# Optimization experiments

Measured on AMD Instinct MI355X. Metric: run time of the kernel, lower is better.

## Reference

```python
import jax, jax.numpy as jnp
import numpy as np
import math

IMG, P, C, D, DEPTH, H, MLP, NCLS, B = 224, 16, 3, 768, 12, 12, 3072, 1000, 32
G = IMG // P          # 14 patches per side
N = G * G             # 196 patches
S = N + 1             # 197 tokens (cls + patches)
DK = D // H
PD = P * P * C        # 768 flattened patch dim


def layer_norm(x, g, b, eps=1e-5):
    mu = jnp.mean(x, axis=-1, keepdims=True)
    var = jnp.mean((x - mu) ** 2, axis=-1, keepdims=True)
    return (x - mu) * jax.lax.rsqrt(var + eps) * g + b


def setup_inputs() -> dict:
    key = jax.random.key(0)
    ks = iter(jax.random.split(key, 32))
    nrm = lambda shape, s=0.02: jax.random.normal(next(ks), shape, jnp.float32) * s
    inp = {
        'x': jax.random.normal(next(ks), (B, C, IMG, IMG), jnp.float32),
        'patch_W': nrm((PD, D)), 'patch_b': jnp.zeros((D,)),
        'cls_token': nrm((1, 1, D)), 'pos_embed': nrm((1, S, D)),
        'Wq': nrm((DEPTH, D, D)), 'bq': jnp.zeros((DEPTH, D)),
        'Wk': nrm((DEPTH, D, D)), 'bk': jnp.zeros((DEPTH, D)),
        'Wv': nrm((DEPTH, D, D)), 'bv': jnp.zeros((DEPTH, D)),
        'Wo': nrm((DEPTH, D, D)), 'bo': jnp.zeros((DEPTH, D)),
        'ln1_g': jnp.ones((DEPTH, D)), 'ln1_b': jnp.zeros((DEPTH, D)),
        'ln2_g': jnp.ones((DEPTH, D)), 'ln2_b': jnp.zeros((DEPTH, D)),
        'W1': nrm((DEPTH, D, MLP)), 'b1': jnp.zeros((DEPTH, MLP)),
        'W2': nrm((DEPTH, MLP, D)), 'b2': jnp.zeros((DEPTH, D)),
        'lnp_g': jnp.ones((D,)), 'lnp_b': jnp.zeros((D,)),
        'head_W': nrm((D, NCLS)), 'head_b': jnp.zeros((NCLS,)),
    }
    return inp


def vit_forward(x, patch_W, patch_b, cls_token, pos_embed,
                Wq, bq, Wk, bk, Wv, bv, Wo, bo,
                ln1_g, ln1_b, ln2_g, ln2_b, W1, b1, W2, b2,
                lnp_g, lnp_b, head_W, head_b):
    b = x.shape[0]
    # faithful replication of torch unfold(2).unfold(3).view: (B,C,G,P,G,P)->(B,C,G,G,P,P)->row-major flatten
    patches = x.reshape(b, C, G, P, G, P).transpose(0, 1, 2, 4, 3, 5).reshape(b, N, PD)
    h = patches @ patch_W + patch_b                              # [B,N,D]
    h = jnp.concatenate([jnp.broadcast_to(cls_token, (b, 1, D)), h], axis=1) + pos_embed
    scale = 1.0 / math.sqrt(DK)
    for i in range(DEPTH):
        y = layer_norm(h, ln1_g[i], ln1_b[i])
        q = (y @ Wq[i] + bq[i]).reshape(b, S, H, DK).transpose(0, 2, 1, 3)
        k = (y @ Wk[i] + bk[i]).reshape(b, S, H, DK).transpose(0, 2, 1, 3)
        v = (y @ Wv[i] + bv[i]).reshape(b, S, H, DK).transpose(0, 2, 1, 3)
        attn = jax.nn.softmax(jnp.einsum('bhqd,bhkd->bhqk', q, k) * scale, axis=-1)
        att = jnp.einsum('bhqk,bhkd->bhqd', attn, v).transpose(0, 2, 1, 3).reshape(b, S, D)
        h = h + att @ Wo[i] + bo[i]
        y = layer_norm(h, ln2_g[i], ln2_b[i])
        h = h + jax.nn.gelu(y @ W1[i] + b1[i], approximate=False) @ W2[i] + b2[i]
    h = layer_norm(h, lnp_g, lnp_b)
    return h[:, 0] @ head_W + head_b                              # [B, NCLS]


def reference(x, patch_W, patch_b, cls_token, pos_embed,
              Wq, bq, Wk, bk, Wv, bv, Wo, bo,
              ln1_g, ln1_b, ln2_g, ln2_b, W1, b1, W2, b2,
              lnp_g, lnp_b, head_W, head_b):
    return vit_forward(x, patch_W, patch_b, cls_token, pos_embed,
                       Wq, bq, Wk, bk, Wv, bv, Wo, bo,
                       ln1_g, ln1_b, ln2_g, ln2_b, W1, b1, W2, b2,
                       lnp_g, lnp_b, head_W, head_b)
```

## Files before the change

### kernel.cpp

```cpp
#include <hip/hip_runtime.h>
#include <hip/hip_bf16.h>


typedef __attribute__((ext_vector_type(8))) short short8;
typedef __attribute__((ext_vector_type(4))) float f32x4;
typedef __attribute__((ext_vector_type(4))) unsigned short us4;

#define MFMA16(a, b, c) __builtin_amdgcn_mfma_f32_16x16x32_bf16(a, b, c, 0, 0, 0)

#define BATCH 32
#define SEQ 197
#define SPAD 208
#define DIM 768
#define HEADS 12
#define DKH 64
#define MLPD 3072
#define NCLS 1000
#define NPATCH 196
#define PDIM 768
#define QKVD 2304
#define ROWS (BATCH * SPAD)

static __device__ __forceinline__ unsigned short f2bf(float f) {
    unsigned int u = __builtin_bit_cast(unsigned int, f);
    u += 0x7fffu + ((u >> 16) & 1u);
    return (unsigned short)(u >> 16);
}

__device__ __forceinline__ void gload16(const void* g, void* l) {
    __builtin_amdgcn_global_load_lds(
        (const __attribute__((address_space(1))) void*)g,
        (__attribute__((address_space(3))) void*)l, 16, 0, 0);
}

__global__ __launch_bounds__(256) void patchify(const float* __restrict__ x,
                                                unsigned short* __restrict__ out) {
    int i = blockIdx.x * 256 + threadIdx.x;
    if (i >= BATCH * NPATCH * PDIM) return;
    int b = i / (NPATCH * PDIM);
    int f = i % (NPATCH * PDIM);
    int c = f / 50176, r = f % 50176;
    int gy = r / 3584, r2 = r % 3584;
    int gx = r2 >> 8, r3 = r2 & 255;
    int py = r3 >> 4, px = r3 & 15;
    float v = x[(((size_t)b * 3 + c) * 224 + gy * 16 + py) * 224 + gx * 16 + px];
    out[i] = f2bf(v);
}

__global__ __launch_bounds__(256) void embed_misc(const float* __restrict__ cls,
                                                  const float* __restrict__ pos,
                                                  float* __restrict__ h) {
    int b = blockIdx.x, t = threadIdx.x;
    float* hb = h + (size_t)b * SPAD * DIM;
    for (int d = t; d < DIM; d += 256) hb[d] = cls[d] + pos[d];
    for (int i = t; i < (SPAD - SEQ) * DIM; i += 256) hb[SEQ * DIM + i] = 0.f;
}

__global__ __launch_bounds__(256) void tconv(const float* __restrict__ src,
                                             unsigned short* __restrict__ dst,
                                             int K, int N) {
    __shared__ float tile[32][33];
    int tn = blockIdx.x, tk = blockIdx.y;
    int t = threadIdx.x, r = t >> 3, c4 = (t & 7) << 2;
    float4 v = *reinterpret_cast<const float4*>(&src[(size_t)(tk * 32 + r) * N + tn * 32 + c4]);
    tile[r][c4 + 0] = v.x; tile[r][c4 + 1] = v.y;
    tile[r][c4 + 2] = v.z; tile[r][c4 + 3] = v.w;
    __syncthreads();
    us4 o = { f2bf(tile[c4 + 0][r]), f2bf(tile[c4 + 1][r]),
              f2bf(tile[c4 + 2][r]), f2bf(tile[c4 + 3][r]) };
    *reinterpret_cast<us4*>(&dst[(size_t)(tn * 32 + r) * K + tk * 32 + c4]) = o;
}

__global__ __launch_bounds__(256) void hconv(const float* __restrict__ src,
                                             unsigned short* __restrict__ dst) {
    __shared__ float tile[32][33];
    int tn = blockIdx.x, tk = blockIdx.y;
    int t = threadIdx.x, r = t >> 3, c4 = (t & 7) << 2;
#pragma unroll
    for (int i = 0; i < 4; ++i) {
        int c = tn * 32 + c4 + i;
        tile[r][c4 + i] = (c < NCLS) ? src[(size_t)(tk * 32 + r) * NCLS + c] : 0.f;
    }
    __syncthreads();
    us4 o = { f2bf(tile[c4 + 0][r]), f2bf(tile[c4 + 1][r]),
              f2bf(tile[c4 + 2][r]), f2bf(tile[c4 + 3][r]) };
    *reinterpret_cast<us4*>(&dst[(size_t)(tn * 32 + r) * 768 + tk * 32 + c4]) = o;
}

__global__ __launch_bounds__(256) void wconvert(const float* __restrict__ q,
                                                const float* __restrict__ k,
                                                const float* __restrict__ v,
                                                const float* __restrict__ o,
                                                const float* __restrict__ w1,
                                                const float* __restrict__ w2,
                                                unsigned short* __restrict__ wT) {
    __shared__ float tile[32][33];
    int tb = blockIdx.x;
    const float* src; unsigned short* dst; int K, N;
    if (tb < 2304) {
        K = 768; N = 768;
        int m = tb / 576; tb -= m * 576;
        src = (m == 0) ? q : (m == 1) ? k : (m == 2) ? v : o;
        dst = wT + (m < 3 ? (size_t)m * 589824 : (size_t)1769472);
    } else if (tb < 4608) {
        tb -= 2304; K = 768; N = 3072; src = w1; dst = wT + 2359296;
    } else {
        tb -= 4608; K = 3072; N = 768; src = w2; dst = wT + 4718592;
    }
    int TN = N >> 5;
    int tn = tb % TN, tk = tb / TN;
    int t = threadIdx.x, r = t >> 3, c4 = (t & 7) << 2;
    float4 vv = *reinterpret_cast<const float4*>(&src[(size_t)(tk * 32 + r) * N + tn * 32 + c4]);
    tile[r][c4 + 0] = vv.x; tile[r][c4 + 1] = vv.y;
    tile[r][c4 + 2] = vv.z; tile[r][c4 + 3] = vv.w;
    __syncthreads();
    us4 ov = { f2bf(tile[c4 + 0][r]), f2bf(tile[c4 + 1][r]),
               f2bf(tile[c4 + 2][r]), f2bf(tile[c4 + 3][r]) };
    *reinterpret_cast<us4*>(&dst[(size_t)(tn * 32 + r) * K + tk * 32 + c4]) = ov;
}

__global__ __launch_bounds__(256) void pack_bias(const float* __restrict__ bq,
                                                 const float* __restrict__ bk,
                                                 const float* __restrict__ bv,
                                                 float* __restrict__ dst) {
    int i = blockIdx.x * 256 + threadIdx.x;
    if (i >= 12 * QKVD) return;
    int l = i / QKVD, c = i % QKVD;
    float v = (c < 768) ? bq[l * 768 + c]
            : (c < 1536) ? bk[l * 768 + c - 768]
                         : bv[l * 768 + c - 1536];
    dst[i] = v;
}

template <int BM>
__global__ __launch_bounds__(256) void gemm_tn(
    const unsigned short* __restrict__ A, const unsigned short* __restrict__ Bt,
    const float* __restrict__ bias, int M, int N, int K, int mode,
    unsigned short* __restrict__ outb, float* __restrict__ outf,
    const float* __restrict__ pos) {
    constexpr int MFRAG = BM / 32;
    constexpr int ACH = BM / 8;
    constexpr int TOT = ACH + 16;
    constexpr int CPW = TOT / 4;
    __shared__ unsigned short Alds[BM * 64];
    __shared__ unsigned short Blds[128 * 64];
    const int tid = threadIdx.x, lane = tid & 63, wid = tid >> 6;
    const int row0 = blockIdx.x * BM, col0 = blockIdx.y * 128;
    const int wm = (wid >> 1) * (BM / 2), wn = (wid & 1) * 64;
    const int lr = lane & 15, lg = lane >> 4;
    const int ric = lane >> 3;
    const int sswz = (lane & 7) ^ ric;

    const char* gptr[CPW];
    char* lptr[CPW];
#pragma unroll
    for (int j = 0; j < CPW; ++j) {
        int cc = wid * CPW + j;
        if (cc < ACH) {
            int grow = row0 + cc * 8 + ric;
            gptr[j] = (const char*)A + (size_t)grow * K * 2 + sswz * 16;
            lptr[j] = (char*)Alds + cc * 1024;
        } else {
            int grow = col0 + (cc - ACH) * 8 + ric;
            gptr[j] = (const char*)Bt + (size_t)grow * K * 2 + sswz * 16;
            lptr[j] = (char*)Blds + (cc - ACH) * 1024;
        }
    }

    f32x4 acc[MFRAG][4];
#pragma unroll
    for (int m = 0; m < MFRAG; ++m)
#pragma unroll
        for (int n = 0; n < 4; ++n) acc[m][n] = (f32x4){0.f, 0.f, 0.f, 0.f};

    const int rsw = lr & 7;
    for (int ks = 0; ks < K; ks += 64) {
        __syncthreads();
#pragma unroll
        for (int j = 0; j < CPW; ++j) {
            gload16(gptr[j], lptr[j]);
            gptr[j] += 128;
        }
        __syncthreads();
        short8 af[MFRAG][2], bfr[4][2];
#pragma unroll
        for (int m = 0; m < MFRAG; ++m)
#pragma unroll
            for (int kk = 0; kk < 2; ++kk)
                af[m][kk] = *reinterpret_cast<const short8*>(
                    &Alds[(wm + m * 16 + lr) * 64 + (((kk * 4 + lg) ^ rsw) << 3)]);
#pragma unroll
        for (int n = 0; n < 4; ++n)
#pragma unroll
            for (int kk = 0; kk < 2; ++kk)
                bfr[n][kk] = *reinterpret_cast<const short8*>(
                    &Blds[(wn + n * 16 + lr) * 64 + (((kk * 4 + lg) ^ rsw) << 3)]);
#pragma unroll
        for (int m = 0; m < MFRAG; ++m)
#pragma unroll
            for (int n = 0; n < 4; ++n) {
                acc[m][n] = MFMA16(af[m][0], bfr[n][0], acc[m][n]);
                acc[m][n] = MFMA16(af[m][1], bfr[n][1], acc[m][n]);
            }
    }
#pragma unroll
    for (int m = 0; m < MFRAG; ++m) {
#pragma unroll
        for (int n = 0; n < 4; ++n) {
            int gcol = col0 + wn + n * 16 + lr;
            float bv = bias ? bias[gcol] : 0.f;
#pragma unroll
            for (int i = 0; i < 4; ++i) {
                int grow = row0 + wm + m * 16 + lg * 4 + i;
                float v = acc[m][n][i] + bv;
                if (mode == 0) {
                    outb[(size_t)grow * N + gcol] = f2bf(v);
                } else if (mode == 1) {
                    outf[(size_t)grow * N + gcol] += v;
                } else if (mode == 2) {
                    v = 0.5f * v * (1.f + erff(v * 0.70710678118654752f));
                    outb[(size_t)grow * N + gcol] = f2bf(v);
                } else if (mode == 3) {
                    int pb = grow / NPATCH, pn = grow % NPATCH;
                    size_t o = ((size_t)pb * SPAD + 1 + pn) * DIM + gcol;
                    outf[o] = v + pos[(size_t)(1 + pn) * DIM + gcol];
                } else {
                    if (grow < BATCH && gcol < NCLS)
                        outf[(size_t)grow * NCLS + gcol] = v + pos[gcol];
                }
            }
        }
    }
}

__global__ __launch_bounds__(256) void ln_bf16(const float* __restrict__ x,
                                               const float* __restrict__ g,
                                               const float* __restrict__ b,
                                               unsigned short* __restrict__ y) {
    __shared__ float red[8];
    int row = blockIdx.x, t = threadIdx.x;
    const float* xr = x + (size_t)row * DIM;
    float v0 = xr[t], v1 = xr[t + 256], v2 = xr[t + 512];
    float s = v0 + v1 + v2, sq = v0 * v0 + v1 * v1 + v2 * v2;
#pragma unroll
    for (int off = 1; off < 64; off <<= 1) {
        s += __shfl_xor(s, off);
        sq += __shfl_xor(sq, off);
    }
    if ((t & 63) == 0) { red[t >> 6] = s; red[4 + (t >> 6)] = sq; }
    __syncthreads();
    s = red[0] + red[1] + red[2] + red[3];
    sq = red[4] + red[5] + red[6] + red[7];
    float mu = s * (1.f / 768.f);
    float var = fmaxf(sq * (1.f / 768.f) - mu * mu, 0.f);
    float rs = rsqrtf(var + 1e-5f);
    unsigned short* yr = y + (size_t)row * DIM;
    yr[t]       = f2bf((v0 - mu) * rs * g[t] + b[t]);
    yr[t + 256] = f2bf((v1 - mu) * rs * g[t + 256] + b[t + 256]);
    yr[t + 512] = f2bf((v2 - mu) * rs * g[t + 512] + b[t + 512]);
}

__global__ __launch_bounds__(256) void ln_cls(const float* __restrict__ x,
                                              const float* __restrict__ g,
                                              const float* __restrict__ b,
                                              unsigned short* __restrict__ y) {
    __shared__ float red[8];
    int bb = blockIdx.x, t = threadIdx.x;
    unsigned short* yr = y + (size_t)bb * DIM;
    if (bb >= BATCH) {
        yr[t] = 0; yr[t + 256] = 0; yr[t + 512] = 0;
        return;
    }
    const float* xr = x + (size_t)bb * SPAD * DIM;
    float v0 = xr[t], v1 = xr[t + 256], v2 = xr[t + 512];
    float s = v0 + v1 + v2, sq = v0 * v0 + v1 * v1 + v2 * v2;
#pragma unroll
    for (int off = 1; off < 64; off <<= 1) {
        s += __shfl_xor(s, off);
        sq += __shfl_xor(sq, off);
    }
    if ((t & 63) == 0) { red[t >> 6] = s; red[4 + (t >> 6)] = sq; }
    __syncthreads();
    s = red[0] + red[1] + red[2] + red[3];
    sq = red[4] + red[5] + red[6] + red[7];
    float mu = s * (1.f / 768.f);
    float var = fmaxf(sq * (1.f / 768.f) - mu * mu, 0.f);
    float rs = rsqrtf(var + 1e-5f);
    yr[t]       = f2bf((v0 - mu) * rs * g[t] + b[t]);
    yr[t + 256] = f2bf((v1 - mu) * rs * g[t + 256] + b[t + 256]);
    yr[t + 512] = f2bf((v2 - mu) * rs * g[t + 512] + b[t + 512]);
}

__global__ __launch_bounds__(256) void attn_fused(const unsigned short* __restrict__ qkv,
                                                  unsigned short* __restrict__ att) {
    __shared__ unsigned short Vlds[64][232];
    __shared__ unsigned short Plds[4][16 * 256];
    int h = blockIdx.x, b = blockIdx.y, tid = threadIdx.x;
    for (int idx = tid; idx < SPAD * 8; idx += 256) {
        int s = idx >> 3, dc = (idx & 7) << 3;
        uint4 w = *reinterpret_cast<const uint4*>(
            &qkv[((size_t)b * SPAD + s) * QKVD + 1536 + h * DKH + dc]);
        const unsigned short* pe = reinterpret_cast<const unsigned short*>(&w);
#pragma unroll
        for (int i = 0; i < 8; ++i) Vlds[dc + i][s] = pe[i];
    }
    for (int i = tid; i < 64 * 24; i += 256) Vlds[i / 24][208 + (i % 24)] = 0;
    __syncthreads();

    int wid = tid >> 6, lane = tid & 63, lr = lane & 15, lg = lane >> 4;
    unsigned short* Pw = &Plds[wid][0];
    const short8 zero8 = {0, 0, 0, 0, 0, 0, 0, 0};

    for (int qt = wid; qt < 13; qt += 4) {
        size_t qoff = ((size_t)b * SPAD + qt * 16 + lr) * QKVD + h * DKH + lg * 8;
        short8 qf0 = *reinterpret_cast<const short8*>(&qkv[qoff]);
        short8 qf1 = *reinterpret_cast<const short8*>(&qkv[qoff + 32]);
        f32x4 acc[13];
#pragma unroll
        for (int kt = 0; kt < 13; ++kt) {
            size_t koff = ((size_t)b * SPAD + kt * 16 + lr) * QKVD + 768 + h * DKH + lg * 8;
            short8 kf0 = *reinterpret_cast<const short8*>(&qkv[koff]);
            short8 kf1 = *reinterpret_cast<const short8*>(&qkv[koff + 32]);
            f32x4 a = (f32x4){0.f, 0.f, 0.f, 0.f};
            a = MFMA16(qf0, kf0, a);
            a = MFMA16(qf1, kf1, a);
            acc[kt] = a;
        }
#pragma unroll
        for (int kt = 0; kt < 13; ++kt)
#pragma unroll
            for (int r = 0; r < 4; ++r) acc[kt][r] *= 0.125f;
        if (lr >= 5) {
#pragma unroll
            for (int r = 0; r < 4; ++r) acc[12][r] = -1e30f;
        }
        float mx[4] = {-1e30f, -1e30f, -1e30f, -1e30f};
#pragma unroll
        for (int kt = 0; kt < 13; ++kt)
#pragma unroll
            for (int r = 0; r < 4; ++r) mx[r] = fmaxf(mx[r], acc[kt][r]);
#pragma unroll
        for (int r = 0; r < 4; ++r) {
            mx[r] = fmaxf(mx[r], __shfl_xor(mx[r], 1));
            mx[r] = fmaxf(mx[r], __shfl_xor(mx[r], 2));
            mx[r] = fmaxf(mx[r], __shfl_xor(mx[r], 4));
            mx[r] = fmaxf(mx[r], __shfl_xor(mx[r], 8));
        }
        float sm[4] = {0.f, 0.f, 0.f, 0.f};
#pragma unroll
        for (int kt = 0; kt < 13; ++kt)
#pragma unroll
            for (int r = 0; r < 4; ++r) {
                float e = __expf(acc[kt][r] - mx[r]);
                acc[kt][r] = e;
                sm[r] += e;
            }
#pragma unroll
        for (int r = 0; r < 4; ++r) {
            sm[r] += __shfl_xor(sm[r], 1);
            sm[r] += __shfl_xor(sm[r], 2);
            sm[r] += __shfl_xor(sm[r], 4);
            sm[r] += __shfl_xor(sm[r], 8);
        }
#pragma unroll
        for (int r = 0; r < 4; ++r) {
            int row = lg * 4 + r;
            float inv = 1.f / sm[r];
#pragma unroll
            for (int kt = 0; kt < 13; ++kt) {
                int col = kt * 16 + lr;
                int idx = row * 256 + ((((col >> 3) ^ (row & 7)) << 3) | (col & 7));
                Pw[idx] = f2bf(acc[kt][r] * inv);
            }
        }
        if (lr < 6) {
            int s = 26 + lr;
#pragma unroll
            for (int r = 0; r < 4; ++r) {
                int row = lg * 4 + r;
                *reinterpret_cast<short8*>(&Pw[row * 256 + ((s ^ (row & 7)) << 3)]) = zero8;
            }
        }
        int rsw = lr & 7;
#pragma unroll
        for (int dt = 0; dt < 4; ++dt) {
            f32x4 a = (f32x4){0.f, 0.f, 0.f, 0.f};
#pragma unroll
            for (int kk = 0; kk < 7; ++kk) {
                short8 af = *reinterpret_cast<const short8*>(
                    &Pw[lr * 256 + (((kk * 4 + lg) ^ rsw) << 3)]);
                short8 bfr = *reinterpret_cast<const short8*>(
                    &Vlds[dt * 16 + lr][kk * 32 + lg * 8]);
                a = MFMA16(af, bfr, a);
            }
#pragma unroll
            for (int i = 0; i < 4; ++i) {
                int s = qt * 16 + lg * 4 + i;
                att[((size_t)b * SPAD + s) * DIM + h * DKH + dt * 16 + lr] = f2bf(a[i]);
            }
        }
    }
}

extern "C" void kernel_launch(void* const* d_in, const int* in_sizes, int n_in,
                              void* d_out, int out_size, void* d_ws, size_t ws_size,
                              hipStream_t stream) {
    const float* x      = (const float*)d_in[0];
    const float* patchW = (const float*)d_in[1];
    const float* patchB = (const float*)d_in[2];
    const float* clstok = (const float*)d_in[3];
    const float* pose   = (const float*)d_in[4];
    const float* Wq = (const float*)d_in[5];
    const float* bq = (const float*)d_in[6];
    const float* Wk = (const float*)d_in[7];
    const float* bk = (const float*)d_in[8];
    const float* Wv = (const float*)d_in[9];
    const float* bv = (const float*)d_in[10];
    const float* Wo = (const float*)d_in[11];
    const float* bo = (const float*)d_in[12];
    const float* ln1g = (const float*)d_in[13];
    const float* ln1b = (const float*)d_in[14];
    const float* ln2g = (const float*)d_in[15];
    const float* ln2b = (const float*)d_in[16];
    const float* W1 = (const float*)d_in[17];
    const float* b1 = (const float*)d_in[18];
    const float* W2 = (const float*)d_in[19];
    const float* b2 = (const float*)d_in[20];
    const float* lnpg = (const float*)d_in[21];
    const float* lnpb = (const float*)d_in[22];
    const float* headW = (const float*)d_in[23];
    const float* headB = (const float*)d_in[24];
    float* out = (float*)d_out;

    constexpr size_t SZ_H   = (size_t)ROWS * DIM * 4;
    constexpr size_t SZ_QKV = (size_t)ROWS * QKVD * 2;
    constexpr size_t SZ_Y   = (size_t)ROWS * DIM * 2;
    constexpr size_t SZ_M1  = (size_t)ROWS * MLPD * 2;
    constexpr size_t SZ_WT  = (size_t)7077888 * 2;
    char* w = (char*)d_ws;
    float* hbuf            = (float*)w;
    unsigned short* qkvb   = (unsigned short*)(w + SZ_H);
    unsigned short* ybuf   = (unsigned short*)(w + SZ_H + SZ_QKV);
    unsigned short* m1buf  = (unsigned short*)(w + SZ_H + SZ_QKV + SZ_Y);
    unsigned short* wT     = (unsigned short*)(w + SZ_H + SZ_QKV + SZ_Y + SZ_M1);
    float* bqkv            = (float*)(w + SZ_H + SZ_QKV + SZ_Y + SZ_M1 + SZ_WT);
    unsigned short* patches = m1buf;
    unsigned short* clsbuf  = m1buf;
    unsigned short* hwT     = m1buf + 64 * DIM;

    pack_bias<<<dim3(108), 256, 0, stream>>>(bq, bk, bv, bqkv);

    tconv<<<dim3(24, 24), 256, 0, stream>>>(patchW, wT, PDIM, DIM);
    patchify<<<dim3((BATCH * NPATCH * PDIM + 255) / 256), 256, 0, stream>>>(x, patches);
    embed_misc<<<dim3(BATCH), 256, 0, stream>>>(clstok, pose, hbuf);
    gemm_tn<64><<<dim3(98, 6), 256, 0, stream>>>(patches, wT, patchB,
                                                 BATCH * NPATCH, DIM, PDIM, 3,
                                                 nullptr, hbuf, pose);

    for (int i = 0; i < 12; ++i) {
        const size_t wo = (size_t)i * DIM * DIM;
        const size_t wm = (size_t)i * DIM * MLPD;
        wconvert<<<dim3(6912), 256, 0, stream>>>(Wq + wo, Wk + wo, Wv + wo, Wo + wo,
                                                 W1 + wm, W2 + wm, wT);
        ln_bf16<<<dim3(ROWS), 256, 0, stream>>>(hbuf, ln1g + i * DIM, ln1b + i * DIM, ybuf);
        gemm_tn<128><<<dim3(52, 18), 256, 0, stream>>>(ybuf, wT, bqkv + i * QKVD,
                                                       ROWS, QKVD, DIM, 0,
                                                       qkvb, nullptr, nullptr);
        attn_fused<<<dim3(HEADS, BATCH), 256, 0, stream>>>(qkvb, ybuf);
        gemm_tn<64><<<dim3(104, 6), 256, 0, stream>>>(ybuf, wT + 1769472, bo + i * DIM,
                                                      ROWS, DIM, DIM, 1,
                                                      nullptr, hbuf, nullptr);
        ln_bf16<<<dim3(ROWS), 256, 0, stream>>>(hbuf, ln2g + i * DIM, ln2b + i * DIM, ybuf);
        gemm_tn<128><<<dim3(52, 24), 256, 0, stream>>>(ybuf, wT + 2359296, b1 + i * MLPD,
                                                       ROWS, MLPD, DIM, 2,
                                                       m1buf, nullptr, nullptr);
        gemm_tn<64><<<dim3(104, 6), 256, 0, stream>>>(m1buf, wT + 4718592, b2 + i * DIM,
                                                      ROWS, DIM, MLPD, 1,
                                                      nullptr, hbuf, nullptr);
    }
    ln_cls<<<dim3(64), 256, 0, stream>>>(hbuf, lnpg, lnpb, clsbuf);
    hconv<<<dim3(32, 24), 256, 0, stream>>>(headW, hwT);
    gemm_tn<64><<<dim3(1, 8), 256, 0, stream>>>(clsbuf, hwT, nullptr,
                                                64, 1024, DIM, 4,
                                                nullptr, out, headB);
}
```

Measured before the change: 3.260 ms.

## Double-buffer GEMM LDS tiles and enlarge block tiles to 128x256 with 8 waves

The GEMM kernel now uses double-buffered shared memory, prefetching the next K-slab while computing on the current one. This removes one barrier per iteration and hides global load latency. Tiles change to a fixed 128-row M tile with a BN of 128 or 256 and 4 or 8 waves, so the QKV and MLP1 GEMMs run 512-thread blocks with 128x256 tiles and the other GEMMs use 128x128. Shared memory use rises, which may lower occupancy, and the head GEMM and ln_cls are resized to match the 128-row tile.

```diff
diff --git a/kernel.cpp b/kernel.cpp
--- a/kernel.cpp
+++ b/kernel.cpp
@@ -132,79 +132,96 @@
     dst[i] = v;
 }
 
-template <int BM>
-__global__ __launch_bounds__(256) void gemm_tn(
+template <int BN, int NW>
+__global__ __launch_bounds__(64 * NW) void gemm_tn(
     const unsigned short* __restrict__ A, const unsigned short* __restrict__ Bt,
     const float* __restrict__ bias, int M, int N, int K, int mode,
     unsigned short* __restrict__ outb, float* __restrict__ outf,
     const float* __restrict__ pos) {
-    constexpr int MFRAG = BM / 32;
-    constexpr int ACH = BM / 8;
-    constexpr int TOT = ACH + 16;
-    constexpr int CPW = TOT / 4;
-    __shared__ unsigned short Alds[BM * 64];
-    __shared__ unsigned short Blds[128 * 64];
+    constexpr int NWN = NW / 2;
+    constexpr int ACH = 16;
+    constexpr int BCH = BN / 8;
+    constexpr int TOT = ACH + BCH;
+    constexpr int CPW = TOT / NW;
+    constexpr int ASZ = 128 * 64;
+    constexpr int BSZ = BN * 64;
+    __shared__ unsigned short Alds[2 * ASZ];
+    __shared__ unsigned short Blds[2 * BSZ];
     const int tid = threadIdx.x, lane = tid & 63, wid = tid >> 6;
-    const int row0 = blockIdx.x * BM, col0 = blockIdx.y * 128;
-    const int wm = (wid >> 1) * (BM / 2), wn = (wid & 1) * 64;
+    const int row0 = blockIdx.x * 128, col0 = blockIdx.y * BN;
+    const int wm = (wid / NWN) * 64, wn = (wid % NWN) * 64;
     const int lr = lane & 15, lg = lane >> 4;
     const int ric = lane >> 3;
     const int sswz = (lane & 7) ^ ric;
 
     const char* gptr[CPW];
-    char* lptr[CPW];
+    char* l0[CPW];
+    int ldelta[CPW];
 #pragma unroll
     for (int j = 0; j < CPW; ++j) {
         int cc = wid * CPW + j;
         if (cc < ACH) {
             int grow = row0 + cc * 8 + ric;
             gptr[j] = (const char*)A + (size_t)grow * K * 2 + sswz * 16;
-            lptr[j] = (char*)Alds + cc * 1024;
+            l0[j] = (char*)Alds + cc * 1024;
+            ldelta[j] = ASZ * 2;
         } else {
             int grow = col0 + (cc - ACH) * 8 + ric;
             gptr[j] = (const char*)Bt + (size_t)grow * K * 2 + sswz * 16;
-            lptr[j] = (char*)Blds + (cc - ACH) * 1024;
-        }
-    }
-
-    f32x4 acc[MFRAG][4];
-#pragma unroll
-    for (int m = 0; m < MFRAG; ++m)
+            l0[j] = (char*)Blds + (cc - ACH) * 1024;
+            ldelta[j] = BSZ * 2;
+        }
+    }
+
+    f32x4 acc[4][4];
+#pragma unroll
+    for (int m = 0; m < 4; ++m)
 #pragma unroll
         for (int n = 0; n < 4; ++n) acc[m][n] = (f32x4){0.f, 0.f, 0.f, 0.f};
 
+#pragma unroll
+    for (int j = 0; j < CPW; ++j) {
+        gload16(gptr[j], l0[j]);
+        gptr[j] += 128;
+    }
+
     const int rsw = lr & 7;
+    int buf = 0;
     for (int ks = 0; ks < K; ks += 64) {
         __syncthreads();
-#pragma unroll
-        for (int j = 0; j < CPW; ++j) {
-            gload16(gptr[j], lptr[j]);
-            gptr[j] += 128;
-        }
-        __syncthreads();
-        short8 af[MFRAG][2], bfr[4][2];
-#pragma unroll
-        for (int m = 0; m < MFRAG; ++m)
+        if (ks + 64 < K) {
+#pragma unroll
+            for (int j = 0; j < CPW; ++j) {
+                gload16(gptr[j], l0[j] + (buf ^ 1) * ldelta[j]);
+                gptr[j] += 128;
+            }
+        }
+        const unsigned short* Ab = Alds + buf * ASZ;
+        const unsigned short* Bb = Blds + buf * BSZ;
+        short8 af[4][2], bfr[4][2];
+#pragma unroll
+        for (int m = 0; m < 4; ++m)
 #pragma unroll
             for (int kk = 0; kk < 2; ++kk)
                 af[m][kk] = *reinterpret_cast<const short8*>(
-                    &Alds[(wm + m * 16 + lr) * 64 + (((kk * 4 + lg) ^ rsw) << 3)]);
+                    &Ab[(wm + m * 16 + lr) * 64 + (((kk * 4 + lg) ^ rsw) << 3)]);
 #pragma unroll
         for (int n = 0; n < 4; ++n)
 #pragma unroll
             for (int kk = 0; kk < 2; ++kk)
                 bfr[n][kk] = *reinterpret_cast<const short8*>(
-                    &Blds[(wn + n * 16 + lr) * 64 + (((kk * 4 + lg) ^ rsw) << 3)]);
-#pragma unroll
-        for (int m = 0; m < MFRAG; ++m)
+                    &Bb[(wn + n * 16 + lr) * 64 + (((kk * 4 + lg) ^ rsw) << 3)]);
+#pragma unroll
+        for (int m = 0; m < 4; ++m)
 #pragma unroll
             for (int n = 0; n < 4; ++n) {
                 acc[m][n] = MFMA16(af[m][0], bfr[n][0], acc[m][n]);
                 acc[m][n] = MFMA16(af[m][1], bfr[n][1], acc[m][n]);
             }
-    }
-#pragma unroll
-    for (int m = 0; m < MFRAG; ++m) {
+        buf ^= 1;
+    }
+#pragma unroll
+    for (int m = 0; m < 4; ++m) {
 #pragma unroll
         for (int n = 0; n < 4; ++n) {
             int gcol = col0 + wn + n * 16 + lr;
@@ -446,16 +463,16 @@
     float* bqkv            = (float*)(w + SZ_H + SZ_QKV + SZ_Y + SZ_M1 + SZ_WT);
     unsigned short* patches = m1buf;
     unsigned short* clsbuf  = m1buf;
-    unsigned short* hwT     = m1buf + 64 * DIM;
+    unsigned short* hwT     = m1buf + 128 * DIM;
 
     pack_bias<<<dim3(108), 256, 0, stream>>>(bq, bk, bv, bqkv);
 
     tconv<<<dim3(24, 24), 256, 0, stream>>>(patchW, wT, PDIM, DIM);
     patchify<<<dim3((BATCH * NPATCH * PDIM + 255) / 256), 256, 0, stream>>>(x, patches);
     embed_misc<<<dim3(BATCH), 256, 0, stream>>>(clstok, pose, hbuf);
-    gemm_tn<64><<<dim3(98, 6), 256, 0, stream>>>(patches, wT, patchB,
-                                                 BATCH * NPATCH, DIM, PDIM, 3,
-                                                 nullptr, hbuf, pose);
+    gemm_tn<128, 4><<<dim3(49, 6), 256, 0, stream>>>(patches, wT, patchB,
+                                                     BATCH * NPATCH, DIM, PDIM, 3,
+                                                     nullptr, hbuf, pose);
 
     for (int i = 0; i < 12; ++i) {
         const size_t wo = (size_t)i * DIM * DIM;
@@ -463,24 +480,24 @@
         wconvert<<<dim3(6912), 256, 0, stream>>>(Wq + wo, Wk + wo, Wv + wo, Wo + wo,
                                                  W1 + wm, W2 + wm, wT);
         ln_bf16<<<dim3(ROWS), 256, 0, stream>>>(hbuf, ln1g + i * DIM, ln1b + i * DIM, ybuf);
-        gemm_tn<128><<<dim3(52, 18), 256, 0, stream>>>(ybuf, wT, bqkv + i * QKVD,
-                                                       ROWS, QKVD, DIM, 0,
-                                                       qkvb, nullptr, nullptr);
+        gemm_tn<256, 8><<<dim3(52, 9), 512, 0, stream>>>(ybuf, wT, bqkv + i * QKVD,
+                                                         ROWS, QKVD, DIM, 0,
+                                                         qkvb, nullptr, nullptr);
         attn_fused<<<dim3(HEADS, BATCH), 256, 0, stream>>>(qkvb, ybuf);
-        gemm_tn<64><<<dim3(104, 6), 256, 0, stream>>>(ybuf, wT + 1769472, bo + i * DIM,
-                                                      ROWS, DIM, DIM, 1,
-                                                      nullptr, hbuf, nullptr);
+        gemm_tn<128, 4><<<dim3(52, 6), 256, 0, stream>>>(ybuf, wT + 1769472, bo + i * DIM,
+                                                         ROWS, DIM, DIM, 1,
+                                                         nullptr, hbuf, nullptr);
         ln_bf16<<<dim3(ROWS), 256, 0, stream>>>(hbuf, ln2g + i * DIM, ln2b + i * DIM, ybuf);
-        gemm_tn<128><<<dim3(52, 24), 256, 0, stream>>>(ybuf, wT + 2359296, b1 + i * MLPD,
-                                                       ROWS, MLPD, DIM, 2,
-                                                       m1buf, nullptr, nullptr);
-        gemm_tn<64><<<dim3(104, 6), 256, 0, stream>>>(m1buf, wT + 4718592, b2 + i * DIM,
-                                                      ROWS, DIM, MLPD, 1,
-                                                      nullptr, hbuf, nullptr);
-    }
-    ln_cls<<<dim3(64), 256, 0, stream>>>(hbuf, lnpg, lnpb, clsbuf);
+        gemm_tn<256, 8><<<dim3(52, 12), 512, 0, stream>>>(ybuf, wT + 2359296, b1 + i * MLPD,
+                                                          ROWS, MLPD, DIM, 2,
+                                                          m1buf, nullptr, nullptr);
+        gemm_tn<128, 4><<<dim3(52, 6), 256, 0, stream>>>(m1buf, wT + 4718592, b2 + i * DIM,
+                                                         ROWS, DIM, MLPD, 1,
+                                                         nullptr, hbuf, nullptr);
+    }
+    ln_cls<<<dim3(128), 256, 0, stream>>>(hbuf, lnpg, lnpb, clsbuf);
     hconv<<<dim3(32, 24), 256, 0, stream>>>(headW, hwT);
-    gemm_tn<64><<<dim3(1, 8), 256, 0, stream>>>(clsbuf, hwT, nullptr,
-                                                64, 1024, DIM, 4,
-                                                nullptr, out, headB);
-}
+    gemm_tn<128, 4><<<dim3(1, 8), 256, 0, stream>>>(clsbuf, hwT, nullptr,
+                                                    128, 1024, DIM, 4,
+                                                    nullptr, out, headB);
+}
```

Measured after the change: 3.577 ms. 1.1x slower.

## Add 256x256 8-wave pipelined GEMM for QKV/MLP1 and stage K in LDS

Applied to the files above, without the earlier changes.

Introduces a 512-thread GEMM kernel with 256x256 tiles, double-buffered direct-to-LDS loads, interleaved prefetch across four MFMA phases, explicit vmcnt waits and setprio. It replaces the 128-row GEMMs used for the QKV and first MLP projections, raising data reuse per tile and overlapping global loads with MFMA work. Separately, attention now loads the K tile into swizzled LDS once per block instead of every wave rereading K from global memory. The larger tile uses 128KB of LDS and many accumulator registers, which may limit occupancy. The grid of 234 or 312 blocks is also fairly coarse for the number of CUs.

```diff
diff --git a/kernel.cpp b/kernel.cpp
--- a/kernel.cpp
+++ b/kernel.cpp
@@ -132,6 +132,140 @@
     dst[i] = v;
 }
 
+#define MM1(MF, J, NF) \
+    acc[MF][NF] = MFMA16(af[J][0], bfr[NF][0], acc[MF][NF]); \
+    acc[MF][NF] = MFMA16(af[J][1], bfr[NF][1], acc[MF][NF]);
+#define MMROW(MF, J) MM1(MF, J, 0) MM1(MF, J, 1) MM1(MF, J, 2) MM1(MF, J, 3)
+
+#define WAITVM(N) \
+    __builtin_amdgcn_sched_barrier(0); \
+    asm volatile("s_waitcnt vmcnt(" #N ")" ::: "memory"); \
+    __builtin_amdgcn_sched_barrier(0);
+
+template <int MODE>
+__global__ __launch_bounds__(512, 2) void gemm8p(
+    const unsigned short* __restrict__ A, const unsigned short* __restrict__ Bt,
+    const float* __restrict__ bias, int N, int K,
+    unsigned short* __restrict__ outb) {
+    __shared__ unsigned short Ab[2][16384];
+    __shared__ unsigned short Bb[2][16384];
+    const int tid = threadIdx.x, lane = tid & 63, wid = tid >> 6;
+    const int wm = wid >> 2, wn = wid & 3;
+    const int lr = lane & 15, lg = lane >> 4;
+    const int ric = lane >> 3, sswz = (lane & 7) ^ ric;
+    const int row0 = blockIdx.x * 256, col0 = blockIdx.y * 256;
+    const char* pA = (const char*)A + ((size_t)(row0 + wid * 8 + ric) * K) * 2 + sswz * 16;
+    const char* pB = (const char*)Bt + ((size_t)(col0 + wid * 8 + ric) * K) * 2 + sswz * 16;
+    const int NT = K >> 6;
+
+    auto stA = [&](int q, int ks, int b) {
+        gload16(pA + ((size_t)q * 64 * K + ks) * 2, (char*)&Ab[b][0] + q * 8192 + wid * 1024);
+    };
+    auto stB = [&](int q, int ks, int b) {
+        gload16(pB + ((size_t)q * 64 * K + ks) * 2, (char*)&Bb[b][0] + q * 8192 + wid * 1024);
+    };
+
+    f32x4 acc[8][4];
+#pragma unroll
+    for (int m = 0; m < 8; ++m)
+#pragma unroll
+        for (int n = 0; n < 4; ++n) acc[m][n] = (f32x4){0.f, 0.f, 0.f, 0.f};
+
+    stB(0, 0, 0); stB(1, 0, 0); stB(2, 0, 0); stB(3, 0, 0);
+    stA(0, 0, 0); stA(2, 0, 0); stA(1, 0, 0); stA(3, 0, 0);
+    if (NT > 1) {
+        stB(0, 64, 1); stB(1, 64, 1); stB(2, 64, 1); stB(3, 64, 1);
+        stA(0, 64, 1); stA(2, 64, 1);
+        WAITVM(4)
+    } else {
+        WAITVM(0)
+    }
+    __builtin_amdgcn_s_barrier();
+
+    const int rsw = lr & 7;
+    for (int s = 0; s < NT; ++s) {
+        const int d = s & 1;
+        const unsigned short* Ad = &Ab[d][0];
+        const unsigned short* Bd = &Bb[d][0];
+        const bool p1ok = (s + 1 < NT), p2ok = (s + 2 < NT);
+        short8 bfr[4][2], af[2][2];
+#pragma unroll
+        for (int nf = 0; nf < 4; ++nf)
+#pragma unroll
+            for (int kk = 0; kk < 2; ++kk)
+                bfr[nf][kk] = *reinterpret_cast<const short8*>(
+                    &Bd[(wn * 64 + nf * 16 + lr) * 64 + (((kk * 4 + lg) ^ rsw) << 3)]);
+#pragma unroll
+        for (int j = 0; j < 2; ++j)
+#pragma unroll
+            for (int kk = 0; kk < 2; ++kk)
+                af[j][kk] = *reinterpret_cast<const short8*>(
+                    &Ad[(wm * 128 + (0 + j) * 16 + lr) * 64 + (((kk * 4 + lg) ^ rsw) << 3)]);
+        if (p1ok) { stA(1, (s + 1) * 64, d ^ 1); stA(3, (s + 1) * 64, d ^ 1); }
+        __builtin_amdgcn_s_barrier();
+        __builtin_amdgcn_s_setprio(1);
+        MMROW(0, 0) MMROW(1, 1)
+        __builtin_amdgcn_s_setprio(0);
+        __builtin_amdgcn_s_barrier();
+#pragma unroll
+        for (int j = 0; j < 2; ++j)
+#pragma unroll
+            for (int kk = 0; kk < 2; ++kk)
+                af[j][kk] = *reinterpret_cast<const short8*>(
+                    &Ad[(wm * 128 + (2 + j) * 16 + lr) * 64 + (((kk * 4 + lg) ^ rsw) << 3)]);
+        if (p2ok) { stB(0, (s + 2) * 64, d); stB(1, (s + 2) * 64, d); }
+        __builtin_amdgcn_s_barrier();
+        __builtin_amdgcn_s_setprio(1);
+        MMROW(2, 0) MMROW(3, 1)
+        __builtin_amdgcn_s_setprio(0);
+        __builtin_amdgcn_s_barrier();
+#pragma unroll
+        for (int j = 0; j < 2; ++j)
+#pragma unroll
+            for (int kk = 0; kk < 2; ++kk)
+                af[j][kk] = *reinterpret_cast<const short8*>(
+                    &Ad[(wm * 128 + (4 + j) * 16 + lr) * 64 + (((kk * 4 + lg) ^ rsw) << 3)]);
+        if (p2ok) { stB(2, (s + 2) * 64, d); stB(3, (s + 2) * 64, d); }
+        __builtin_amdgcn_s_barrier();
+        __builtin_amdgcn_s_setprio(1);
+        MMROW(4, 0) MMROW(5, 1)
+        __builtin_amdgcn_s_setprio(0);
+        __builtin_amdgcn_s_barrier();
+#pragma unroll
+        for (int j = 0; j < 2; ++j)
+#pragma unroll
+            for (int kk = 0; kk < 2; ++kk)
+                af[j][kk] = *reinterpret_cast<const short8*>(
+                    &Ad[(wm * 128 + (6 + j) * 16 + lr) * 64 + (((kk * 4 + lg) ^ rsw) << 3)]);
+        if (p2ok) {
+            stA(0, (s + 2) * 64, d); stA(2, (s + 2) * 64, d);
+            WAITVM(4)
+        } else {
+            WAITVM(0)
+        }
+        __builtin_amdgcn_s_barrier();
+        __builtin_amdgcn_s_setprio(1);
+        MMROW(6, 0) MMROW(7, 1)
+        __builtin_amdgcn_s_setprio(0);
+        __builtin_amdgcn_s_barrier();
+    }
+#pragma unroll
+    for (int m = 0; m < 8; ++m) {
+#pragma unroll
+        for (int n = 0; n < 4; ++n) {
+            int gcol = col0 + wn * 64 + n * 16 + lr;
+            float bv = bias[gcol];
+#pragma unroll
+            for (int i = 0; i < 4; ++i) {
+                int grow = row0 + wm * 128 + m * 16 + lg * 4 + i;
+                float v = acc[m][n][i] + bv;
+                if (MODE == 2) v = 0.5f * v * (1.f + erff(v * 0.70710678118654752f));
+                outb[(size_t)grow * N + gcol] = f2bf(v);
+            }
+        }
+    }
+}
+
 template <int BM>
 __global__ __launch_bounds__(256) void gemm_tn(
     const unsigned short* __restrict__ A, const unsigned short* __restrict__ Bt,
@@ -293,9 +427,18 @@
 
 __global__ __launch_bounds__(256) void attn_fused(const unsigned short* __restrict__ qkv,
                                                   unsigned short* __restrict__ att) {
+    __shared__ unsigned short Klds[26 * 512];
     __shared__ unsigned short Vlds[64][232];
     __shared__ unsigned short Plds[4][16 * 256];
     int h = blockIdx.x, b = blockIdx.y, tid = threadIdx.x;
+    int wid = tid >> 6, lane = tid & 63, lr = lane & 15, lg = lane >> 4;
+    const int ric = lane >> 3, sswz = (lane & 7) ^ ric;
+
+    const char* pK = (const char*)qkv +
+        ((size_t)(b * SPAD + ric) * QKVD + 768 + h * DKH) * 2 + sswz * 16;
+    for (int c = wid; c < 26; c += 4)
+        gload16(pK + (size_t)c * 8 * QKVD * 2, (char*)Klds + c * 1024);
+
     for (int idx = tid; idx < SPAD * 8; idx += 256) {
         int s = idx >> 3, dc = (idx & 7) << 3;
         uint4 w = *reinterpret_cast<const uint4*>(
@@ -307,9 +450,9 @@
     for (int i = tid; i < 64 * 24; i += 256) Vlds[i / 24][208 + (i % 24)] = 0;
     __syncthreads();
 
-    int wid = tid >> 6, lane = tid & 63, lr = lane & 15, lg = lane >> 4;
     unsigned short* Pw = &Plds[wid][0];
     const short8 zero8 = {0, 0, 0, 0, 0, 0, 0, 0};
+    const int rowin = lr & 7;
 
     for (int qt = wid; qt < 13; qt += 4) {
         size_t qoff = ((size_t)b * SPAD + qt * 16 + lr) * QKVD + h * DKH + lg * 8;
@@ -318,9 +461,9 @@
         f32x4 acc[13];
 #pragma unroll
         for (int kt = 0; kt < 13; ++kt) {
-            size_t koff = ((size_t)b * SPAD + kt * 16 + lr) * QKVD + 768 + h * DKH + lg * 8;
-            short8 kf0 = *reinterpret_cast<const short8*>(&qkv[koff]);
-            short8 kf1 = *reinterpret_cast<const short8*>(&qkv[koff + 32]);
+            const unsigned short* kbase = Klds + (kt * 2 + (lr >> 3)) * 512 + rowin * 64;
+            short8 kf0 = *reinterpret_cast<const short8*>(&kbase[(lg ^ rowin) << 3]);
+            short8 kf1 = *reinterpret_cast<const short8*>(&kbase[((4 + lg) ^ rowin) << 3]);
             f32x4 a = (f32x4){0.f, 0.f, 0.f, 0.f};
             a = MFMA16(qf0, kf0, a);
             a = MFMA16(qf1, kf1, a);
@@ -463,17 +606,15 @@
         wconvert<<<dim3(6912), 256, 0, stream>>>(Wq + wo, Wk + wo, Wv + wo, Wo + wo,
                                                  W1 + wm, W2 + wm, wT);
         ln_bf16<<<dim3(ROWS), 256, 0, stream>>>(hbuf, ln1g + i * DIM, ln1b + i * DIM, ybuf);
-        gemm_tn<128><<<dim3(52, 18), 256, 0, stream>>>(ybuf, wT, bqkv + i * QKVD,
-                                                       ROWS, QKVD, DIM, 0,
-                                                       qkvb, nullptr, nullptr);
+        gemm8p<0><<<dim3(26, 9), 512, 0, stream>>>(ybuf, wT, bqkv + i * QKVD,
+                                                   QKVD, DIM, qkvb);
         attn_fused<<<dim3(HEADS, BATCH), 256, 0, stream>>>(qkvb, ybuf);
         gemm_tn<64><<<dim3(104, 6), 256, 0, stream>>>(ybuf, wT + 1769472, bo + i * DIM,
                                                       ROWS, DIM, DIM, 1,
                                                       nullptr, hbuf, nullptr);
         ln_bf16<<<dim3(ROWS), 256, 0, stream>>>(hbuf, ln2g + i * DIM, ln2b + i * DIM, ybuf);
-        gemm_tn<128><<<dim3(52, 24), 256, 0, stream>>>(ybuf, wT + 2359296, b1 + i * MLPD,
-                                                       ROWS, MLPD, DIM, 2,
-                                                       m1buf, nullptr, nullptr);
+        gemm8p<2><<<dim3(26, 12), 512, 0, stream>>>(ybuf, wT + 2359296, b1 + i * MLPD,
+                                                    MLPD, DIM, m1buf);
         gemm_tn<64><<<dim3(104, 6), 256, 0, stream>>>(m1buf, wT + 4718592, b2 + i * DIM,
                                                       ROWS, DIM, MLPD, 1,
                                                       nullptr, hbuf, nullptr);
```

Result: faster. 3.044 ms (-6.6%).
